# Optimization experiments

Measured on AMD Instinct MI355X. Metric: run time of the kernel, lower is better.

Reference implementation:

```python
import jax, jax.numpy as jnp
import numpy as np

N_NODES = 50000
N_EDGES = 800000
HEADS = 4
OUT_C = 64
NEG_SLOPE = 0.2


def setup_inputs() -> dict:
    key = jax.random.key(0)
    k1, k2, k3, k4 = jax.random.split(key, 4)
    x = jax.random.normal(k1, (N_NODES, OUT_C), dtype=jnp.float32)
    edge_index = jax.random.randint(k2, (2, N_EDGES), 0, N_NODES, dtype=jnp.int64)
    # Glorot-ish scaling for stability
    W = jax.random.normal(k3, (OUT_C, HEADS * OUT_C), dtype=jnp.float32) * (1.0 / np.sqrt(OUT_C))
    att = jax.random.normal(k4, (HEADS, OUT_C), dtype=jnp.float32) * (1.0 / np.sqrt(OUT_C))
    bias = jnp.zeros((HEADS * OUT_C,), dtype=jnp.float32)
    return {"x": x, "edge_index": edge_index, "W": W, "att": att, "bias": bias}


def _gatv2(x, edge_index, W, att, bias):
    N = x.shape[0]
    src, dst = edge_index[0], edge_index[1]
    # shared weights: x_l == x_r
    xl = (x @ W).reshape(N, HEADS, OUT_C)  # [N,H,C]
    feat = xl[src] + xl[dst]               # [E,H,C] per-edge gather
    feat = jnp.where(feat > 0, feat, NEG_SLOPE * feat)  # LeakyReLU
    score = jnp.einsum('ehc,hc->eh', feat, att)          # [E,H]
    # segment softmax over destination nodes
    smax = jax.ops.segment_max(score, dst, num_segments=N)  # [N,H]
    smax = jnp.where(jnp.isfinite(smax), smax, 0.0)
    ex = jnp.exp(score - smax[dst])                          # [E,H]
    denom = jax.ops.segment_sum(ex, dst, num_segments=N)     # [N,H]
    denom = jnp.where(denom > 0, denom, 1.0)
    alpha = ex / denom[dst]                                  # [E,H]
    msg = alpha[:, :, None] * xl[src]                        # [E,H,C]
    out = jax.ops.segment_sum(msg, dst, num_segments=N)      # [N,H,C]
    out = out.reshape(N, HEADS * OUT_C) + bias
    return jax.nn.relu(out)


def reference(x, edge_index, W, att, bias):
    return _gatv2(x, edge_index, W, att, bias)
```

## Files before the change

kernel.cpp:

```cpp
#include <hip/hip_runtime.h>
#include <math.h>

#define N_NODES 50000
#define N_EDGES 800000
#define HEADS 4
#define OUT_C 64
#define HC 256
#define NEG_SLOPE 0.2f
#define NBUCKET 196
#define CHUNK 1000
#define NBLK 800
#define WT_BLOCKS 64
#define GEMM_BLOCKS (N_NODES / 16)
#define LOG2E 1.44269504f

typedef __attribute__((ext_vector_type(8))) short bf16x8;
typedef __attribute__((ext_vector_type(4))) float f32x4;

__device__ inline unsigned short f2bf(float f) {
    unsigned u = __float_as_uint(f);
    return (unsigned short)((u + 0x7FFFu + ((u >> 16) & 1u)) >> 16);
}
__device__ inline float bf2f(unsigned short h) {
    return __uint_as_float(((unsigned)h) << 16);
}

__device__ inline float rowsum16(float p) {
    int y;
    y = __builtin_amdgcn_update_dpp(0, __float_as_int(p), 0x121, 0xF, 0xF, false);
    p += __int_as_float(y);
    y = __builtin_amdgcn_update_dpp(0, __float_as_int(p), 0x122, 0xF, 0xF, false);
    p += __int_as_float(y);
    y = __builtin_amdgcn_update_dpp(0, __float_as_int(p), 0x124, 0xF, 0xF, false);
    p += __int_as_float(y);
    y = __builtin_amdgcn_update_dpp(0, __float_as_int(p), 0x128, 0xF, 0xF, false);
    p += __int_as_float(y);
    return p;
}

__global__ void k_hist1(const int* __restrict__ dst, int* __restrict__ M,
                        const float* __restrict__ W, unsigned short* __restrict__ Wt,
                        int* __restrict__ done) {
    int b = blockIdx.x, t = threadIdx.x;
    if (b >= NBLK) {
        if (b == NBLK && t == 0) *done = 0;
        int idx = (b - NBLK) * 256 + t;
        int c = idx >> 6, k = idx & 63;
        Wt[idx] = f2bf(W[(size_t)k * HC + c]);
        return;
    }
    __shared__ int h[NBUCKET];
    if (t < NBUCKET) h[t] = 0;
    __syncthreads();
    int base = b * CHUNK;
    for (int i = base + t; i < base + CHUNK; i += 256)
        atomicAdd(&h[dst[i] >> 8], 1);
    __syncthreads();
    if (t < NBUCKET) M[(size_t)t * NBLK + b] = h[t];
}

__global__ void k_scan2(int* __restrict__ M, int* __restrict__ coarse,
                        int* __restrict__ coarseBase, int* __restrict__ rowL,
                        int* __restrict__ ssorted, int* __restrict__ done) {
    __shared__ int wsum[4];
    __shared__ int carry_s, tot_s, lastflag;
    int b = blockIdx.x, t = threadIdx.x;
    int lane = t & 63, w = t >> 6;
    if (t == 0) carry_s = 0;
    __syncthreads();
    int* Mrow = M + (size_t)b * NBLK;
    for (int c0 = 0; c0 < NBLK; c0 += 256) {
        int idx = c0 + t;
        int v = (idx < NBLK) ? Mrow[idx] : 0;
        int x = v;
        #pragma unroll
        for (int off = 1; off < 64; off <<= 1) {
            int y = __shfl_up(x, off);
            if (lane >= off) x += y;
        }
        if (lane == 63) wsum[w] = x;
        __syncthreads();
        if (t == 0) {
            int s0 = wsum[0], s1 = wsum[1], s2 = wsum[2], s3 = wsum[3];
            wsum[0] = 0; wsum[1] = s0; wsum[2] = s0 + s1; wsum[3] = s0 + s1 + s2;
            tot_s = s0 + s1 + s2 + s3;
        }
        __syncthreads();
        int excl = x - v + wsum[w] + carry_s;
        if (idx < NBLK) Mrow[idx] = excl;
        __syncthreads();
        if (t == 0) carry_s += tot_s;
        __syncthreads();
    }
    if (t == 0) coarse[b] = carry_s;
    __threadfence();
    if (t == 0) lastflag = (atomicAdd(done, 1) == NBUCKET - 1);
    __syncthreads();
    if (!lastflag) return;
    if (t == 0) *done = 0;
    __threadfence();
    int v = (t < NBUCKET) ? coarse[t] : 0;
    int x = v;
    #pragma unroll
    for (int off = 1; off < 64; off <<= 1) {
        int y = __shfl_up(x, off);
        if (lane >= off) x += y;
    }
    if (lane == 63) wsum[w] = x;
    __syncthreads();
    if (t == 0) {
        int s0 = wsum[0], s1 = wsum[1], s2 = wsum[2];
        wsum[0] = 0; wsum[1] = s0; wsum[2] = s0 + s1; wsum[3] = s0 + s1 + s2;
    }
    __syncthreads();
    int excl = x - v + wsum[w];
    if (t < NBUCKET) coarseBase[t] = excl;
    if (t == NBUCKET - 1) coarseBase[NBUCKET] = excl + v;
    if (t == 0) rowL[N_NODES] = N_EDGES;
    if (t < 16) ssorted[N_EDGES + t] = 0;
}

__global__ __launch_bounds__(256) void k_scatter_gemm(
    const int* __restrict__ src, const int* __restrict__ dst,
    const int* __restrict__ M, const int* __restrict__ coarseBase,
    int* __restrict__ tmp,
    const float* __restrict__ x, const unsigned short* __restrict__ Wt,
    unsigned short* __restrict__ xlh) {
    int b = blockIdx.x, t = threadIdx.x;
    if (b < NBLK) {
        __shared__ int cur[NBUCKET];
        if (t < NBUCKET) cur[t] = coarseBase[t] + M[(size_t)t * NBLK + b];
        __syncthreads();
        int base = b * CHUNK;
        for (int i = base + t; i < base + CHUNK; i += 256) {
            int d = dst[i];
            int pos = atomicAdd(&cur[d >> 8], 1);
            tmp[pos] = ((d & 255) << 16) | src[i];
        }
        return;
    }
    int wv = t >> 6, l = t & 63;
    int row0 = (b - NBLK) * 16;
    int r = l & 15, kg = l >> 4, ko = kg * 8;
    const float* xrow = x + (size_t)(row0 + r) * OUT_C;
    f32x4 a0 = *(const f32x4*)(xrow + ko);
    f32x4 a1 = *(const f32x4*)(xrow + ko + 4);
    f32x4 a2 = *(const f32x4*)(xrow + 32 + ko);
    f32x4 a3 = *(const f32x4*)(xrow + 32 + ko + 4);
    bf16x8 A0, A1;
    #pragma unroll
    for (int j = 0; j < 4; ++j) {
        A0[j]     = (short)f2bf(a0[j]);
        A0[j + 4] = (short)f2bf(a1[j]);
        A1[j]     = (short)f2bf(a2[j]);
        A1[j + 4] = (short)f2bf(a3[j]);
    }
    int drow = kg * 4;
    #pragma unroll
    for (int i = 0; i < 4; ++i) {
        int c0 = wv * 16 + i * 64;
        const unsigned short* wp = Wt + (size_t)(c0 + r) * OUT_C + ko;
        bf16x8 B0 = *(const bf16x8*)(wp);
        bf16x8 B1 = *(const bf16x8*)(wp + 32);
        f32x4 acc = {0.f, 0.f, 0.f, 0.f};
        acc = __builtin_amdgcn_mfma_f32_16x16x32_bf16(A0, B0, acc, 0, 0, 0);
        acc = __builtin_amdgcn_mfma_f32_16x16x32_bf16(A1, B1, acc, 0, 0, 0);
        #pragma unroll
        for (int j = 0; j < 4; ++j)
            xlh[(size_t)(row0 + drow + j) * HC + c0 + r] = f2bf(acc[j]);
    }
}

__global__ void k_csr(const int* __restrict__ tmp, const int* __restrict__ coarseBase,
                      int* __restrict__ rowL, int* __restrict__ ssorted) {
    __shared__ int h[256];
    __shared__ int cur[256];
    __shared__ int wsum[4];
    int b = blockIdx.x, t = threadIdx.x;
    int lane = t & 63, w = t >> 6;
    int s = coarseBase[b], e = coarseBase[b + 1];
    h[t] = 0;
    __syncthreads();
    for (int i = s + t; i < e; i += 256)
        atomicAdd(&h[(tmp[i] >> 16) & 255], 1);
    __syncthreads();
    int v = h[t];
    int x = v;
    #pragma unroll
    for (int off = 1; off < 64; off <<= 1) {
        int y = __shfl_up(x, off);
        if (lane >= off) x += y;
    }
    if (lane == 63) wsum[w] = x;
    __syncthreads();
    if (t == 0) {
        int s0 = wsum[0], s1 = wsum[1], s2 = wsum[2];
        wsum[0] = 0; wsum[1] = s0; wsum[2] = s0 + s1; wsum[3] = s0 + s1 + s2;
    }
    __syncthreads();
    int excl = x - v + wsum[w];
    int n = b * 256 + t;
    if (n < N_NODES) rowL[n] = s + excl;
    cur[t] = s + excl;
    __syncthreads();
    for (int i = s + t; i < e; i += 256) {
        int p = tmp[i];
        int pos = atomicAdd(&cur[(p >> 16) & 255], 1);
        ssorted[pos] = p & 0xFFFF;
    }
}

__global__ __launch_bounds__(256) void k_node(
    const unsigned short* __restrict__ xlh, const int* __restrict__ rowL,
    const int* __restrict__ ssorted, const float* __restrict__ att,
    const float* __restrict__ bias, float* __restrict__ out) {
    int w = threadIdx.x >> 6;
    int lane = threadIdx.x & 63;
    int n = blockIdx.x * 4 + w;
    int start = __builtin_amdgcn_readfirstlane(rowL[n]);
    int end   = __builtin_amdgcn_readfirstlane(rowL[n + 1]);
    int ne = end - start;
    const int* sp = ssorted + start;
    int c4 = lane << 2;
    const unsigned short* xp = xlh + c4;
    ushort4 xq = *(const ushort4*)(xp + (size_t)n * HC);
    float4 xn = make_float4(bf2f(xq.x), bf2f(xq.y), bf2f(xq.z), bf2f(xq.w));
    float4 at = *(const float4*)(att + c4);
    float4 at6 = make_float4(at.x * (0.6f * LOG2E), at.y * (0.6f * LOG2E),
                             at.z * (0.6f * LOG2E), at.w * (0.6f * LOG2E));
    float4 at4 = make_float4(at.x * (0.4f * LOG2E), at.y * (0.4f * LOG2E),
                             at.z * (0.4f * LOG2E), at.w * (0.4f * LOG2E));
    float4 acc = make_float4(0.f, 0.f, 0.f, 0.f);
    float den = 0.0f;

#define EDGE(vq) {                                                        \
        float4 vc = make_float4(bf2f(vq.x), bf2f(vq.y),                   \
                                bf2f(vq.z), bf2f(vq.w));                  \
        float f, p;                                                       \
        f = xn.x + vc.x; p  = f * at6.x + fabsf(f) * at4.x;               \
        f = xn.y + vc.y; p += f * at6.y + fabsf(f) * at4.y;               \
        f = xn.z + vc.z; p += f * at6.z + fabsf(f) * at4.z;               \
        f = xn.w + vc.w; p += f * at6.w + fabsf(f) * at4.w;               \
        p = rowsum16(p);                                                  \
        float ex = exp2f(p);                                              \
        den += ex;                                                        \
        acc.x += ex * vc.x; acc.y += ex * vc.y;                           \
        acc.z += ex * vc.z; acc.w += ex * vc.w; }

    if (ne > 0) {
        int sa = sp[0];
        int sb = sp[1];
        ushort4 va = *(const ushort4*)(xp + (size_t)sa * HC);
        ushort4 vb = *(const ushort4*)(xp + (size_t)sb * HC);
        sa = sp[2];
        sb = sp[3];
        int i = 0;
        for (; i + 1 < ne; i += 2) {
            ushort4 v0 = va, v1 = vb;
            va = *(const ushort4*)(xp + (size_t)sa * HC);
            vb = *(const ushort4*)(xp + (size_t)sb * HC);
            sa = sp[i + 4];
            sb = sp[i + 5];
            EDGE(v0);
            EDGE(v1);
        }
        if (i < ne) EDGE(va);
    }
#undef EDGE

    float r = 1.0f / (den > 0.0f ? den : 1.0f);
    const float4 b4 = *(const float4*)(bias + c4);
    float4 o;
    o.x = fmaxf(acc.x * r + b4.x, 0.0f);
    o.y = fmaxf(acc.y * r + b4.y, 0.0f);
    o.z = fmaxf(acc.z * r + b4.z, 0.0f);
    o.w = fmaxf(acc.w * r + b4.w, 0.0f);
    *(float4*)(out + (size_t)n * HC + c4) = o;
}

extern "C" void kernel_launch(void* const* d_in, const int* in_sizes, int n_in,
                              void* d_out, int out_size, void* d_ws, size_t ws_size,
                              hipStream_t stream) {
    const float* x    = (const float*)d_in[0];
    const int*   edge = (const int*)d_in[1];
    const float* W    = (const float*)d_in[2];
    const float* att  = (const float*)d_in[3];
    const float* bias = (const float*)d_in[4];
    float* out = (float*)d_out;

    const int* src = edge;
    const int* dst = edge + N_EDGES;

    char* ws = (char*)d_ws;
    unsigned short* xlh = (unsigned short*)ws;
    unsigned short* Wt  = (unsigned short*)(ws + 25600000);
    int* M          = (int*)(ws + 25632768);
    int* coarse     = (int*)(ws + 26259968);
    int* coarseBase = (int*)(ws + 26260800);
    int* done       = (int*)(ws + 26261632);
    int* rowL       = (int*)(ws + 26261696);
    int* tmp        = (int*)(ws + 26461760);
    int* ssorted    = (int*)(ws + 29661760);

    k_hist1<<<NBLK + WT_BLOCKS, 256, 0, stream>>>(dst, M, W, Wt, done);
    k_scan2<<<NBUCKET, 256, 0, stream>>>(M, coarse, coarseBase, rowL, ssorted, done);
    k_scatter_gemm<<<NBLK + GEMM_BLOCKS, 256, 0, stream>>>(src, dst, M, coarseBase,
                                                           tmp, x, Wt, xlh);
    k_csr<<<NBUCKET, 256, 0, stream>>>(tmp, coarseBase, rowL, ssorted);
    k_node<<<N_NODES / 4, 256, 0, stream>>>(xlh, rowL, ssorted, att, bias, out);
}
```

Baseline: 133.6 us.

## Quantize projected node features to per-row int8 to halve gather traffic

The GEMM epilogue now computes a per-row absolute max via shared-memory atomics and stores xl as offset uint8 with a per-row float scale, instead of bf16. The node kernel gathers 4 bytes per lane plus one scale per edge, reconstructs features, and subtracts the self term algebraically at the end. This halves the bytes moved in the random gather over 800k edges and the xl write. In exchange it loses precision (8-bit), adds an extra scale load per edge, and adds a sync in the GEMM epilogue.

```diff
diff --git a/kernel.cpp b/kernel.cpp
--- a/kernel.cpp
+++ b/kernel.cpp
@@ -21,9 +21,11 @@
     unsigned u = __float_as_uint(f);
     return (unsigned short)((u + 0x7FFFu + ((u >> 16) & 1u)) >> 16);
 }
-__device__ inline float bf2f(unsigned short h) {
-    return __uint_as_float(((unsigned)h) << 16);
-}
+
+__device__ inline float ub0(unsigned q) { return (float)(q & 0xFFu); }
+__device__ inline float ub1(unsigned q) { return (float)((q >> 8) & 0xFFu); }
+__device__ inline float ub2(unsigned q) { return (float)((q >> 16) & 0xFFu); }
+__device__ inline float ub3(unsigned q) { return (float)(q >> 24); }
 
 __device__ inline float rowsum16(float p) {
     int y;
@@ -125,10 +127,11 @@
     const int* __restrict__ M, const int* __restrict__ coarseBase,
     int* __restrict__ tmp,
     const float* __restrict__ x, const unsigned short* __restrict__ Wt,
-    unsigned short* __restrict__ xlh) {
+    unsigned char* __restrict__ xq, float* __restrict__ scl) {
+    __shared__ int shmem[NBUCKET];
     int b = blockIdx.x, t = threadIdx.x;
     if (b < NBLK) {
-        __shared__ int cur[NBUCKET];
+        int* cur = shmem;
         if (t < NBUCKET) cur[t] = coarseBase[t] + M[(size_t)t * NBLK + b];
         __syncthreads();
         int base = b * CHUNK;
@@ -139,6 +142,7 @@
         }
         return;
     }
+    int* rmax = shmem;
     int wv = t >> 6, l = t & 63;
     int row0 = (b - NBLK) * 16;
     int r = l & 15, kg = l >> 4, ko = kg * 8;
@@ -155,20 +159,38 @@
         A1[j]     = (short)f2bf(a2[j]);
         A1[j + 4] = (short)f2bf(a3[j]);
     }
+    if (t < 16) rmax[t] = __float_as_int(1e-6f);
+    __syncthreads();
+    f32x4 acc0 = {0,0,0,0}, acc1 = {0,0,0,0}, acc2 = {0,0,0,0}, acc3 = {0,0,0,0};
+#define DO_TILE(ACC, I) {                                                     \
+        const unsigned short* wp = Wt + (size_t)(wv * 16 + (I) * 64 + r) * OUT_C + ko; \
+        bf16x8 B0 = *(const bf16x8*)(wp);                                     \
+        bf16x8 B1 = *(const bf16x8*)(wp + 32);                                \
+        ACC = __builtin_amdgcn_mfma_f32_16x16x32_bf16(A0, B0, ACC, 0, 0, 0);  \
+        ACC = __builtin_amdgcn_mfma_f32_16x16x32_bf16(A1, B1, ACC, 0, 0, 0); }
+    DO_TILE(acc0, 0) DO_TILE(acc1, 1) DO_TILE(acc2, 2) DO_TILE(acc3, 3)
+#undef DO_TILE
     int drow = kg * 4;
     #pragma unroll
-    for (int i = 0; i < 4; ++i) {
-        int c0 = wv * 16 + i * 64;
-        const unsigned short* wp = Wt + (size_t)(c0 + r) * OUT_C + ko;
-        bf16x8 B0 = *(const bf16x8*)(wp);
-        bf16x8 B1 = *(const bf16x8*)(wp + 32);
-        f32x4 acc = {0.f, 0.f, 0.f, 0.f};
-        acc = __builtin_amdgcn_mfma_f32_16x16x32_bf16(A0, B0, acc, 0, 0, 0);
-        acc = __builtin_amdgcn_mfma_f32_16x16x32_bf16(A1, B1, acc, 0, 0, 0);
-        #pragma unroll
-        for (int j = 0; j < 4; ++j)
-            xlh[(size_t)(row0 + drow + j) * HC + c0 + r] = f2bf(acc[j]);
-    }
+    for (int j = 0; j < 4; ++j) {
+        float m = fmaxf(fmaxf(fabsf(acc0[j]), fabsf(acc1[j])),
+                        fmaxf(fabsf(acc2[j]), fabsf(acc3[j])));
+        atomicMax(&rmax[drow + j], __float_as_int(m));
+    }
+    __syncthreads();
+    float is[4];
+    #pragma unroll
+    for (int j = 0; j < 4; ++j)
+        is[j] = 127.0f / __int_as_float(rmax[drow + j]);
+    #pragma unroll
+    for (int j = 0; j < 4; ++j) {
+        size_t base = (size_t)(row0 + drow + j) * HC + r;
+        xq[base + wv * 16 + 0 * 64] = (unsigned char)((int)rintf(acc0[j] * is[j]) + 128);
+        xq[base + wv * 16 + 1 * 64] = (unsigned char)((int)rintf(acc1[j] * is[j]) + 128);
+        xq[base + wv * 16 + 2 * 64] = (unsigned char)((int)rintf(acc2[j] * is[j]) + 128);
+        xq[base + wv * 16 + 3 * 64] = (unsigned char)((int)rintf(acc3[j] * is[j]) + 128);
+    }
+    if (t < 16) scl[row0 + t] = __int_as_float(rmax[t]) * (1.0f / 127.0f);
 }
 
 __global__ void k_csr(const int* __restrict__ tmp, const int* __restrict__ coarseBase,
@@ -211,9 +233,10 @@
 }
 
 __global__ __launch_bounds__(256) void k_node(
-    const unsigned short* __restrict__ xlh, const int* __restrict__ rowL,
-    const int* __restrict__ ssorted, const float* __restrict__ att,
-    const float* __restrict__ bias, float* __restrict__ out) {
+    const unsigned char* __restrict__ xq, const float* __restrict__ scl,
+    const int* __restrict__ rowL, const int* __restrict__ ssorted,
+    const float* __restrict__ att, const float* __restrict__ bias,
+    float* __restrict__ out) {
     int w = threadIdx.x >> 6;
     int lane = threadIdx.x & 63;
     int n = blockIdx.x * 4 + w;
@@ -222,59 +245,72 @@
     int ne = end - start;
     const int* sp = ssorted + start;
     int c4 = lane << 2;
-    const unsigned short* xp = xlh + c4;
-    ushort4 xq = *(const ushort4*)(xp + (size_t)n * HC);
-    float4 xn = make_float4(bf2f(xq.x), bf2f(xq.y), bf2f(xq.z), bf2f(xq.w));
+    const unsigned char* xp = xq + c4;
+    float sn = scl[n];
+    float offn = 128.0f * sn;
+    unsigned qn = *(const unsigned*)(xp + (size_t)n * HC);
+    float4 xn;
+    xn.x = ub0(qn) * sn - offn;
+    xn.y = ub1(qn) * sn - offn;
+    xn.z = ub2(qn) * sn - offn;
+    xn.w = ub3(qn) * sn - offn;
     float4 at = *(const float4*)(att + c4);
     float4 at6 = make_float4(at.x * (0.6f * LOG2E), at.y * (0.6f * LOG2E),
                              at.z * (0.6f * LOG2E), at.w * (0.6f * LOG2E));
     float4 at4 = make_float4(at.x * (0.4f * LOG2E), at.y * (0.4f * LOG2E),
                              at.z * (0.4f * LOG2E), at.w * (0.4f * LOG2E));
-    float4 acc = make_float4(0.f, 0.f, 0.f, 0.f);
+    float4 accf = make_float4(0.f, 0.f, 0.f, 0.f);
     float den = 0.0f;
 
-#define EDGE(vq) {                                                        \
-        float4 vc = make_float4(bf2f(vq.x), bf2f(vq.y),                   \
-                                bf2f(vq.z), bf2f(vq.w));                  \
-        float f, p;                                                       \
-        f = xn.x + vc.x; p  = f * at6.x + fabsf(f) * at4.x;               \
-        f = xn.y + vc.y; p += f * at6.y + fabsf(f) * at4.y;               \
-        f = xn.z + vc.z; p += f * at6.z + fabsf(f) * at4.z;               \
-        f = xn.w + vc.w; p += f * at6.w + fabsf(f) * at4.w;               \
+#define EDGE(qv, sv) {                                                    \
+        float xo_x = xn.x - 128.0f * sv, xo_y = xn.y - 128.0f * sv;       \
+        float xo_z = xn.z - 128.0f * sv, xo_w = xn.w - 128.0f * sv;       \
+        float f0 = ub0(qv) * sv + xo_x;                                   \
+        float f1 = ub1(qv) * sv + xo_y;                                   \
+        float f2 = ub2(qv) * sv + xo_z;                                   \
+        float f3 = ub3(qv) * sv + xo_w;                                   \
+        float p;                                                          \
+        p  = f0 * at6.x + fabsf(f0) * at4.x;                              \
+        p += f1 * at6.y + fabsf(f1) * at4.y;                              \
+        p += f2 * at6.z + fabsf(f2) * at4.z;                              \
+        p += f3 * at6.w + fabsf(f3) * at4.w;                              \
         p = rowsum16(p);                                                  \
         float ex = exp2f(p);                                              \
         den += ex;                                                        \
-        acc.x += ex * vc.x; acc.y += ex * vc.y;                           \
-        acc.z += ex * vc.z; acc.w += ex * vc.w; }
+        accf.x += ex * f0; accf.y += ex * f1;                             \
+        accf.z += ex * f2; accf.w += ex * f3; }
 
     if (ne > 0) {
         int sa = sp[0];
         int sb = sp[1];
-        ushort4 va = *(const ushort4*)(xp + (size_t)sa * HC);
-        ushort4 vb = *(const ushort4*)(xp + (size_t)sb * HC);
+        unsigned qa = *(const unsigned*)(xp + (size_t)sa * HC);
+        unsigned qb = *(const unsigned*)(xp + (size_t)sb * HC);
+        float ssa = scl[sa], ssb = scl[sb];
         sa = sp[2];
         sb = sp[3];
         int i = 0;
         for (; i + 1 < ne; i += 2) {
-            ushort4 v0 = va, v1 = vb;
-            va = *(const ushort4*)(xp + (size_t)sa * HC);
-            vb = *(const ushort4*)(xp + (size_t)sb * HC);
+            unsigned q0 = qa, q1 = qb;
+            float s0 = ssa, s1 = ssb;
+            qa = *(const unsigned*)(xp + (size_t)sa * HC);
+            qb = *(const unsigned*)(xp + (size_t)sb * HC);
+            ssa = scl[sa]; ssb = scl[sb];
             sa = sp[i + 4];
             sb = sp[i + 5];
-            EDGE(v0);
-            EDGE(v1);
+            EDGE(q0, s0);
+            EDGE(q1, s1);
         }
-        if (i < ne) EDGE(va);
+        if (i < ne) EDGE(qa, ssa);
     }
 #undef EDGE
 
     float r = 1.0f / (den > 0.0f ? den : 1.0f);
-    const float4 b4 = *(const float4*)(bias + c4);
+    float4 b4 = *(const float4*)(bias + c4);
     float4 o;
-    o.x = fmaxf(acc.x * r + b4.x, 0.0f);
-    o.y = fmaxf(acc.y * r + b4.y, 0.0f);
-    o.z = fmaxf(acc.z * r + b4.z, 0.0f);
-    o.w = fmaxf(acc.w * r + b4.w, 0.0f);
+    o.x = fmaxf((accf.x - xn.x * den) * r + b4.x, 0.0f);
+    o.y = fmaxf((accf.y - xn.y * den) * r + b4.y, 0.0f);
+    o.z = fmaxf((accf.z - xn.z * den) * r + b4.z, 0.0f);
+    o.w = fmaxf((accf.w - xn.w * den) * r + b4.w, 0.0f);
     *(float4*)(out + (size_t)n * HC + c4) = o;
 }
 
@@ -292,20 +328,21 @@
     const int* dst = edge + N_EDGES;
 
     char* ws = (char*)d_ws;
-    unsigned short* xlh = (unsigned short*)ws;
-    unsigned short* Wt  = (unsigned short*)(ws + 25600000);
-    int* M          = (int*)(ws + 25632768);
-    int* coarse     = (int*)(ws + 26259968);
-    int* coarseBase = (int*)(ws + 26260800);
-    int* done       = (int*)(ws + 26261632);
-    int* rowL       = (int*)(ws + 26261696);
-    int* tmp        = (int*)(ws + 26461760);
-    int* ssorted    = (int*)(ws + 29661760);
+    unsigned char* xq  = (unsigned char*)ws;
+    float* scl      = (float*)(ws + 12800000);
+    unsigned short* Wt = (unsigned short*)(ws + 13000000);
+    int* M          = (int*)(ws + 13032768);
+    int* coarse     = (int*)(ws + 13659968);
+    int* coarseBase = (int*)(ws + 13660800);
+    int* done       = (int*)(ws + 13661632);
+    int* rowL       = (int*)(ws + 13661696);
+    int* tmp        = (int*)(ws + 13861760);
+    int* ssorted    = (int*)(ws + 17061760);
 
     k_hist1<<<NBLK + WT_BLOCKS, 256, 0, stream>>>(dst, M, W, Wt, done);
     k_scan2<<<NBUCKET, 256, 0, stream>>>(M, coarse, coarseBase, rowL, ssorted, done);
     k_scatter_gemm<<<NBLK + GEMM_BLOCKS, 256, 0, stream>>>(src, dst, M, coarseBase,
-                                                           tmp, x, Wt, xlh);
+                                                           tmp, x, Wt, xq, scl);
     k_csr<<<NBUCKET, 256, 0, stream>>>(tmp, coarseBase, rowL, ssorted);
-    k_node<<<N_NODES / 4, 256, 0, stream>>>(xlh, rowL, ssorted, att, bias, out);
-}
+    k_node<<<N_NODES / 4, 256, 0, stream>>>(xq, scl, rowL, ssorted, att, bias, out);
+}
```

New measurement: 131.2 us (median of 2 runs). No clear change (-1.8%).
